# Kernel tuning notes

Hardware: AMD Instinct MI355X
Metric: run time of the kernel (lower is better)

The kernel has to match this reference:

```python
import jax, jax.numpy as jnp
import numpy as np

N, K, CIN, COUT = 1_000_000, 27, 32, 32  # active voxels, 3^3 kernel offsets, channels
EPS = 1e-5


def setup_inputs() -> dict:
    key = jax.random.key(0)
    k0, k1, k2, k3 = jax.random.split(key, 4)
    feats = jax.random.normal(k0, (N, CIN), jnp.float32)
    # per-kernel-offset weight matrices, Kaiming-ish scale
    W = jax.random.normal(k1, (K, CIN, COUT), jnp.float32) * (1.0 / np.sqrt(K * CIN))
    gamma = jnp.ones((COUT,), jnp.float32)
    beta = jnp.zeros((COUT,), jnp.float32)
    # precomputed sparse-conv neighbor map: index of input voxel contributing
    nbr_idx = jax.random.randint(k2, (N, K), 0, N, jnp.int32)
    nbr_mask = jax.random.bernoulli(k3, 0.5, (N, K))
    return {"feats": feats, "W": W, "gamma": gamma, "beta": beta,
            "nbr_idx": nbr_idx, "nbr_mask": nbr_mask}


def _sparse_conv(feats, W, nbr_idx, nbr_mask):
    # gather-GEMM-scatter, looped over the small fixed kernel volume (27)
    # to avoid materializing an [N, 27, CIN] gathered tensor.
    acc = jnp.zeros((feats.shape[0], W.shape[2]), feats.dtype)
    for k in range(W.shape[0]):
        g = jnp.where(nbr_mask[:, k, None], feats[nbr_idx[:, k]], 0.0)  # [N, CIN]
        acc = acc + g @ W[k]  # [N, COUT]
    return acc


def reference(feats, W, gamma, beta, nbr_idx, nbr_mask):
    y = _sparse_conv(feats, W, nbr_idx, nbr_mask)           # conv (bias=False, bn=True)
    mean = jnp.mean(y, axis=0)                              # MinkowskiBatchNorm (batch stats)
    var = jnp.mean(jnp.square(y - mean), axis=0)
    y = (y - mean) * jax.lax.rsqrt(var + EPS) * gamma + beta
    return jax.nn.relu(y)                                   # MinkowskiReLU
```

## Files before the change

### kernel.cpp

```cpp
#include <hip/hip_runtime.h>

typedef _Float16 half8 __attribute__((ext_vector_type(8)));
typedef float floatx4 __attribute__((ext_vector_type(4)));

#define CIN 32
#define COUT 32
#define KOFF 27
#define EPSV 1e-5f


__global__ void setup_k(const float* __restrict__ W, _Float16* __restrict__ wp,
                        const unsigned char* __restrict__ m,
                        int* __restrict__ flag) {
  if (blockIdx.x < KOFF) {
    int ko = blockIdx.x;
    int h = threadIdx.x >> 6;
    int lane = threadIdx.x & 63;
    int col = lane & 15, quad = lane >> 4;
    half8 p;
#pragma unroll
    for (int j = 0; j < 8; ++j) {
      int k = quad * 8 + j;
      p[j] = (_Float16)W[(ko * CIN + k) * COUT + h * 16 + col];
    }
    *(half8*)(wp + ((size_t)(ko * 2 + h) * 64 + lane) * 8) = p;
  } else {
    int tid = threadIdx.x;
    int any = 0;
    for (int i = tid; i < 4096; i += 128) {
      if ((i & 3) != 0 && m[i] != 0) any = 1;
    }
    if (any) atomicOr(flag, 1);
  }
}

__global__ void prep_k(const float* __restrict__ feats,
                       _Float16* __restrict__ f16, int total8) {
  int t = blockIdx.x * 256 + threadIdx.x;
  if (t < total8) {
    const floatx4* in4 = (const floatx4*)feats;
    floatx4 a = __builtin_nontemporal_load(&in4[(size_t)t * 2]);
    floatx4 b = __builtin_nontemporal_load(&in4[(size_t)t * 2 + 1]);
    half8 h;
    h[0] = (_Float16)a[0]; h[1] = (_Float16)a[1];
    h[2] = (_Float16)a[2]; h[3] = (_Float16)a[3];
    h[4] = (_Float16)b[0]; h[5] = (_Float16)b[1];
    h[6] = (_Float16)b[2]; h[7] = (_Float16)b[3];
    *(half8*)(f16 + (size_t)t * 8) = h;
  } else if (t < total8 + 4) {
    half8 z;
#pragma unroll
    for (int j = 0; j < 8; ++j) z[j] = (_Float16)0.f;
    *(half8*)(f16 + (size_t)t * 8) = z;
  }
}

__launch_bounds__(256, 4)
__global__ void conv_mfma_l(const _Float16* __restrict__ f16,
                            const _Float16* __restrict__ wp,
                            const int* __restrict__ nidx,
                            const unsigned char* __restrict__ nmask,
                            const int* __restrict__ flagp,
                            float* __restrict__ y,
                            float* __restrict__ stats, int N) {
  __shared__ int lidx[4 * 64 * KOFF];
  __shared__ float smS[4 * 32];
  __shared__ float smQ[4 * 32];
  int wave = threadIdx.x >> 6;
  int lane = threadIdx.x & 63;
  int base = (blockIdx.x * 4 + wave) * 64;
  bool active = base < N;
  int col = lane & 15, quad = lane >> 4;
  const half8* wfrag = (const half8*)wp;
  const _Float16* fq = f16 + quad * 8;
  int* lw = lidx + wave * (64 * KOFF);

  floatx4 acc[4][2];
#pragma unroll
  for (int t = 0; t < 4; ++t)
#pragma unroll
    for (int h = 0; h < 2; ++h) {
      acc[t][h][0] = 0.f; acc[t][h][1] = 0.f;
      acc[t][h][2] = 0.f; acc[t][h][3] = 0.f;
    }

  if (active) {
    bool bytemode = (*flagp != 0);
    int nv = N - base; if (nv > 64) nv = 64;
    if (nv == 64) {
      const int4* gi = (const int4*)(nidx + (size_t)base * KOFF);
      const int4* gm4 = (const int4*)((const int*)nmask + (size_t)base * KOFF);
      const unsigned int* gmb = (const unsigned int*)(nmask + (size_t)base * KOFF);
#pragma unroll
      for (int s = 0; s < 7; ++s) {
        int id4 = s * 64 + lane;
        if (id4 < 432) {
          int4 iv = gi[id4];
          unsigned int m0, m1, m2, m3;
          if (bytemode) {
            unsigned int mw = gmb[id4];
            m0 = mw & 0xffu; m1 = mw & 0xff00u;
            m2 = mw & 0xff0000u; m3 = mw & 0xff000000u;
          } else {
            int4 mv = gm4[id4];
            m0 = (unsigned int)mv.x; m1 = (unsigned int)mv.y;
            m2 = (unsigned int)mv.z; m3 = (unsigned int)mv.w;
          }
          int4 ov;
          ov.x = (iv.x & 0x7FFFFFFF) | (m0 ? (int)0x80000000 : 0);
          ov.y = (iv.y & 0x7FFFFFFF) | (m1 ? (int)0x80000000 : 0);
          ov.z = (iv.z & 0x7FFFFFFF) | (m2 ? (int)0x80000000 : 0);
          ov.w = (iv.w & 0x7FFFFFFF) | (m3 ? (int)0x80000000 : 0);
          *(int4*)(lw + id4 * 4) = ov;
        }
      }
    } else {
      int total = nv * KOFF;
      for (int p = lane; p < total; p += 64) {
        size_t g = (size_t)base * KOFF + p;
        int iv = nidx[g];
        int mk = bytemode ? (int)nmask[g] : ((const int*)nmask)[g];
        lw[p] = (iv & 0x7FFFFFFF) | (mk ? (int)0x80000000 : 0);
      }
      for (int p = nv * KOFF + lane; p < 64 * KOFF; p += 64) lw[p] = 0;
    }

    half8 aC[4];
    int ivB[4];
#pragma unroll
    for (int t = 0; t < 4; ++t) {
      int v0 = lw[(t * 16 + col) * KOFF + 0];
      int sel = (v0 < 0) ? (v0 & 0x7FFFFFFF) : N;
      aC[t] = *(const half8*)(fq + ((size_t)sel << 5));
      ivB[t] = lw[(t * 16 + col) * KOFF + 1];
    }
    half8 bC0 = wfrag[lane];
    half8 bC1 = wfrag[64 + lane];

#pragma unroll
    for (int ko = 0; ko < KOFF; ++ko) {
      half8 aN[4];
      half8 bN0, bN1;
      int ivN[4];
      if (ko + 1 < KOFF) {
        bN0 = wfrag[(size_t)((ko + 1) * 2 + 0) * 64 + lane];
        bN1 = wfrag[(size_t)((ko + 1) * 2 + 1) * 64 + lane];
#pragma unroll
        for (int t = 0; t < 4; ++t) {
          int v = ivB[t];
          int sel = (v < 0) ? (v & 0x7FFFFFFF) : N;
          aN[t] = *(const half8*)(fq + ((size_t)sel << 5));
        }
      }
      if (ko + 2 < KOFF) {
#pragma unroll
        for (int t = 0; t < 4; ++t)
          ivN[t] = lw[(t * 16 + col) * KOFF + ko + 2];
      }
#pragma unroll
      for (int t = 0; t < 4; ++t) {
        acc[t][0] = __builtin_amdgcn_mfma_f32_16x16x32_f16(aC[t], bC0, acc[t][0], 0, 0, 0);
        acc[t][1] = __builtin_amdgcn_mfma_f32_16x16x32_f16(aC[t], bC1, acc[t][1], 0, 0, 0);
      }
      if (ko + 1 < KOFF) {
#pragma unroll
        for (int t = 0; t < 4; ++t) aC[t] = aN[t];
        bC0 = bN0; bC1 = bN1;
      }
      if (ko + 2 < KOFF) {
#pragma unroll
        for (int t = 0; t < 4; ++t) ivB[t] = ivN[t];
      }
    }
  }

  float s0 = 0.f, s1 = 0.f, q0 = 0.f, q1 = 0.f;
  if (active) {
#pragma unroll
    for (int t = 0; t < 4; ++t) {
#pragma unroll
      for (int h = 0; h < 2; ++h) {
        floatx4 c = acc[t][h];
        int co = h * 16 + col;
#pragma unroll
        for (int r = 0; r < 4; ++r) {
          int vox = base + t * 16 + quad * 4 + r;
          if (vox < N) {
            y[(size_t)vox * COUT + co] = c[r];
            float v = c[r];
            if (h == 0) { s0 += v; q0 += v * v; }
            else        { s1 += v; q1 += v * v; }
          }
        }
      }
    }
  }
  s0 += __shfl_xor(s0, 16); s0 += __shfl_xor(s0, 32);
  s1 += __shfl_xor(s1, 16); s1 += __shfl_xor(s1, 32);
  q0 += __shfl_xor(q0, 16); q0 += __shfl_xor(q0, 32);
  q1 += __shfl_xor(q1, 16); q1 += __shfl_xor(q1, 32);
  if (quad == 0) {
    smS[wave * 32 + col] = s0;
    smS[wave * 32 + 16 + col] = s1;
    smQ[wave * 32 + col] = q0;
    smQ[wave * 32 + 16 + col] = q1;
  }
  __syncthreads();
  int tid = threadIdx.x;
  if (tid < 64) {
    int co = tid & 31;
    const float* arr = (tid < 32) ? smS : smQ;
    float s = arr[co] + arr[32 + co] + arr[64 + co] + arr[96 + co];
    atomicAdd(&stats[(tid < 32 ? 0 : 32) + co], s);
  }
}

__global__ void bn_apply(float* __restrict__ y, const float* __restrict__ stats,
                         const float* __restrict__ gamma,
                         const float* __restrict__ beta, int total4, float invN) {
  __shared__ float sc_sh[64];
  int tid = threadIdx.x;
  if (tid < 32) {
    float mean = stats[tid] * invN;
    float ex2 = stats[32 + tid] * invN;
    float var = ex2 - mean * mean;
    float inv = rsqrtf(var + EPSV);
    float sc = gamma[tid] * inv;
    sc_sh[tid] = sc;
    sc_sh[32 + tid] = beta[tid] - mean * sc;
  }
  __syncthreads();
  int t = blockIdx.x * blockDim.x + tid;
  if (t >= total4) return;
  size_t g = (size_t)t * 4;
  int co = (int)(g & 31);
  floatx4 v = *(const floatx4*)(y + g);
  floatx4 sc = *(const floatx4*)&sc_sh[co];
  floatx4 sh = *(const floatx4*)&sc_sh[32 + co];
  floatx4 o;
#pragma unroll
  for (int j = 0; j < 4; ++j) o[j] = fmaxf(0.f, v[j] * sc[j] + sh[j]);
  __builtin_nontemporal_store(o, (floatx4*)(y + g));
}

extern "C" void kernel_launch(void* const* d_in, const int* in_sizes, int n_in,
                              void* d_out, int out_size, void* d_ws,
                              size_t ws_size, hipStream_t stream) {
  const float* feats = (const float*)d_in[0];
  const float* W = (const float*)d_in[1];
  const float* gamma = (const float*)d_in[2];
  const float* beta = (const float*)d_in[3];
  const int* nidx = (const int*)d_in[4];
  const unsigned char* nmask = (const unsigned char*)d_in[5];
  float* out = (float*)d_out;

  int N = in_sizes[0] / CIN;

  char* ws = (char*)d_ws;
  size_t f16_bytes = (size_t)(N + 1) * CIN * sizeof(_Float16);
  _Float16* f16 = (_Float16*)ws;
  _Float16* wp = (_Float16*)(ws + f16_bytes);
  size_t wp_bytes = (size_t)KOFF * 2 * 64 * 8 * sizeof(_Float16);
  size_t stats_off = ((f16_bytes + wp_bytes + 511) / 512) * 512;
  float* stats = (float*)(ws + stats_off);
  int* flag = (int*)(stats + 64);

  hipMemsetAsync(stats, 0, 65 * sizeof(float), stream);

  setup_k<<<KOFF + 1, 128, 0, stream>>>(W, wp, nmask, flag);

  int total8 = N * CIN / 8;
  int cvtBlocks = (total8 + 4 + 255) / 256;
  prep_k<<<cvtBlocks, 256, 0, stream>>>(feats, f16, total8);

  int nwaves = (N + 63) / 64;
  int nblocks = (nwaves + 3) / 4;
  conv_mfma_l<<<nblocks, 256, 0, stream>>>(f16, wp, nidx, nmask, flag, out,
                                           stats, N);

  int total4 = N * COUT / 4;
  bn_apply<<<(total4 + 255) / 256, 256, 0, stream>>>(out, stats, gamma, beta,
                                                     total4, 1.0f / (float)N);
}
```

Before: 623.1 us.

## Stage gathered neighbor features through swizzled LDS with row-contiguous lane mapping

Each group of four lanes now gathers the four 16-byte chunks of one neighbor voxel row, so each row is read contiguously by adjacent lanes. The rows are written into a per-wave XOR-swizzled LDS buffer and read back in the MFMA A-fragment layout. This targets gather coalescing in the neighbor load. In exchange it adds LDS writes and reads per kernel offset, about 16 KB more shared memory per block with launch bounds lowered to 3, and it drops the register prefetch of weight fragments.

```diff
diff --git a/kernel.cpp b/kernel.cpp
--- a/kernel.cpp
+++ b/kernel.cpp
@@ -55,8 +55,8 @@
   }
 }
 
-__launch_bounds__(256, 4)
-__global__ void conv_mfma_l(const _Float16* __restrict__ f16,
+__launch_bounds__(256, 3)
+__global__ void conv_mfma_q(const _Float16* __restrict__ f16,
                             const _Float16* __restrict__ wp,
                             const int* __restrict__ nidx,
                             const unsigned char* __restrict__ nmask,
@@ -64,6 +64,7 @@
                             float* __restrict__ y,
                             float* __restrict__ stats, int N) {
   __shared__ int lidx[4 * 64 * KOFF];
+  __shared__ _Float16 sstage[4 * 64 * 32];
   __shared__ float smS[4 * 32];
   __shared__ float smQ[4 * 32];
   int wave = threadIdx.x >> 6;
@@ -72,8 +73,8 @@
   bool active = base < N;
   int col = lane & 15, quad = lane >> 4;
   const half8* wfrag = (const half8*)wp;
-  const _Float16* fq = f16 + quad * 8;
   int* lw = lidx + wave * (64 * KOFF);
+  _Float16* stg = sstage + wave * (64 * 32);
 
   floatx4 acc[4][2];
 #pragma unroll
@@ -125,37 +126,49 @@
       for (int p = nv * KOFF + lane; p < 64 * KOFF; p += 64) lw[p] = 0;
     }
 
-    half8 aC[4];
+    int vg_sub = lane >> 2;
+    int cch = lane & 3;
+    int swz_w = cch ^ ((lane >> 2) & 3) ^ ((lane >> 4) & 3);
+    int swz_r = quad ^ (col & 3) ^ (col >> 2);
+    const _Float16* fch = f16 + cch * 8;
+
+    half8 gv[4];
     int ivB[4];
 #pragma unroll
-    for (int t = 0; t < 4; ++t) {
-      int v0 = lw[(t * 16 + col) * KOFF + 0];
+    for (int i = 0; i < 4; ++i) {
+      int v0 = lw[(16 * i + vg_sub) * KOFF + 0];
       int sel = (v0 < 0) ? (v0 & 0x7FFFFFFF) : N;
-      aC[t] = *(const half8*)(fq + ((size_t)sel << 5));
-      ivB[t] = lw[(t * 16 + col) * KOFF + 1];
-    }
-    half8 bC0 = wfrag[lane];
-    half8 bC1 = wfrag[64 + lane];
+      gv[i] = *(const half8*)(fch + ((size_t)sel << 5));
+    }
+#pragma unroll
+    for (int i = 0; i < 4; ++i) ivB[i] = lw[(16 * i + vg_sub) * KOFF + 1];
+#pragma unroll
+    for (int i = 0; i < 4; ++i)
+      *(half8*)(stg + (16 * i + vg_sub) * 32 + swz_w * 8) = gv[i];
 
 #pragma unroll
     for (int ko = 0; ko < KOFF; ++ko) {
-      half8 aN[4];
-      half8 bN0, bN1;
-      int ivN[4];
+      half8 aC[4];
+#pragma unroll
+      for (int t = 0; t < 4; ++t)
+        aC[t] = *(const half8*)(stg + (t * 16 + col) * 32 + swz_r * 8);
+      half8 bC0 = wfrag[(size_t)(ko * 2 + 0) * 64 + lane];
+      half8 bC1 = wfrag[(size_t)(ko * 2 + 1) * 64 + lane];
       if (ko + 1 < KOFF) {
-        bN0 = wfrag[(size_t)((ko + 1) * 2 + 0) * 64 + lane];
-        bN1 = wfrag[(size_t)((ko + 1) * 2 + 1) * 64 + lane];
-#pragma unroll
-        for (int t = 0; t < 4; ++t) {
-          int v = ivB[t];
+#pragma unroll
+        for (int i = 0; i < 4; ++i) {
+          int v = ivB[i];
           int sel = (v < 0) ? (v & 0x7FFFFFFF) : N;
-          aN[t] = *(const half8*)(fq + ((size_t)sel << 5));
+          gv[i] = *(const half8*)(fch + ((size_t)sel << 5));
         }
       }
       if (ko + 2 < KOFF) {
-#pragma unroll
-        for (int t = 0; t < 4; ++t)
-          ivN[t] = lw[(t * 16 + col) * KOFF + ko + 2];
+        int ivN[4];
+#pragma unroll
+        for (int i = 0; i < 4; ++i)
+          ivN[i] = lw[(16 * i + vg_sub) * KOFF + ko + 2];
+#pragma unroll
+        for (int i = 0; i < 4; ++i) ivB[i] = ivN[i];
       }
 #pragma unroll
       for (int t = 0; t < 4; ++t) {
@@ -164,12 +177,8 @@
       }
       if (ko + 1 < KOFF) {
 #pragma unroll
-        for (int t = 0; t < 4; ++t) aC[t] = aN[t];
-        bC0 = bN0; bC1 = bN1;
-      }
-      if (ko + 2 < KOFF) {
-#pragma unroll
-        for (int t = 0; t < 4; ++t) ivB[t] = ivN[t];
+        for (int i = 0; i < 4; ++i)
+          *(half8*)(stg + (16 * i + vg_sub) * 32 + swz_w * 8) = gv[i];
       }
     }
   }
@@ -275,7 +284,7 @@
 
   int nwaves = (N + 63) / 64;
   int nblocks = (nwaves + 3) / 4;
-  conv_mfma_l<<<nblocks, 256, 0, stream>>>(f16, wp, nidx, nmask, flag, out,
+  conv_mfma_q<<<nblocks, 256, 0, stream>>>(f16, wp, nidx, nmask, flag, out,
                                            stats, N);
 
   int total4 = N * COUT / 4;
```

New measurement: 615.1 us. Within noise of the previous version (-1.3%).

## Store conv output as fp16 intermediate, fuse prep kernels, nontemporal index loads

Applied to the files above, without the earlier changes.

The conv kernel now writes its pre-normalization output as fp16 to a workspace buffer instead of fp32 into the output, and the BN/ReLU pass reads those fp16 values and writes fp32 output. This halves the intermediate write and read traffic. The weight packing, mask-format probe, stats zeroing and feature conversion are merged into one launch, removing a memset and a kernel launch. Neighbor index and mask loads become nontemporal. The fp16 intermediate loses precision before normalization, while the batch statistics are still computed in fp32.

```diff
diff --git a/kernel.cpp b/kernel.cpp
--- a/kernel.cpp
+++ b/kernel.cpp
@@ -2,6 +2,7 @@
 
 typedef _Float16 half8 __attribute__((ext_vector_type(8)));
 typedef float floatx4 __attribute__((ext_vector_type(4)));
+typedef int intx4 __attribute__((ext_vector_type(4)));
 
 #define CIN 32
 #define COUT 32
@@ -9,34 +10,46 @@
 #define EPSV 1e-5f
 
 
-__global__ void setup_k(const float* __restrict__ W, _Float16* __restrict__ wp,
-                        const unsigned char* __restrict__ m,
-                        int* __restrict__ flag) {
-  if (blockIdx.x < KOFF) {
-    int ko = blockIdx.x;
-    int h = threadIdx.x >> 6;
-    int lane = threadIdx.x & 63;
-    int col = lane & 15, quad = lane >> 4;
-    half8 p;
-#pragma unroll
-    for (int j = 0; j < 8; ++j) {
-      int k = quad * 8 + j;
-      p[j] = (_Float16)W[(ko * CIN + k) * COUT + h * 16 + col];
-    }
-    *(half8*)(wp + ((size_t)(ko * 2 + h) * 64 + lane) * 8) = p;
-  } else {
-    int tid = threadIdx.x;
+__global__ void fused_prep(const float* __restrict__ feats,
+                           _Float16* __restrict__ f16, int total8,
+                           const float* __restrict__ W,
+                           _Float16* __restrict__ wp,
+                           const unsigned char* __restrict__ m,
+                           int* __restrict__ flag,
+                           float* __restrict__ stats) {
+  int bx = blockIdx.x;
+  int tid = threadIdx.x;
+  if (bx < KOFF) {
+    if (tid < 128) {
+      int ko = bx;
+      int h = tid >> 6;
+      int lane = tid & 63;
+      int col = lane & 15, quad = lane >> 4;
+      half8 p;
+#pragma unroll
+      for (int j = 0; j < 8; ++j) {
+        int k = quad * 8 + j;
+        p[j] = (_Float16)W[(ko * CIN + k) * COUT + h * 16 + col];
+      }
+      *(half8*)(wp + ((size_t)(ko * 2 + h) * 64 + lane) * 8) = p;
+    }
+    return;
+  }
+  if (bx == KOFF) {
+    __shared__ int red;
+    if (tid == 0) red = 0;
+    __syncthreads();
     int any = 0;
-    for (int i = tid; i < 4096; i += 128) {
+    for (int i = tid; i < 4096; i += 256) {
       if ((i & 3) != 0 && m[i] != 0) any = 1;
     }
-    if (any) atomicOr(flag, 1);
-  }
-}
-
-__global__ void prep_k(const float* __restrict__ feats,
-                       _Float16* __restrict__ f16, int total8) {
-  int t = blockIdx.x * 256 + threadIdx.x;
+    if (any) atomicOr(&red, 1);
+    __syncthreads();
+    if (tid == 0) *flag = red;
+    if (tid < 64) stats[tid] = 0.f;
+    return;
+  }
+  int t = (bx - KOFF - 1) * 256 + tid;
   if (t < total8) {
     const floatx4* in4 = (const floatx4*)feats;
     floatx4 a = __builtin_nontemporal_load(&in4[(size_t)t * 2]);
@@ -61,7 +74,7 @@
                             const int* __restrict__ nidx,
                             const unsigned char* __restrict__ nmask,
                             const int* __restrict__ flagp,
-                            float* __restrict__ y,
+                            _Float16* __restrict__ y16,
                             float* __restrict__ stats, int N) {
   __shared__ int lidx[4 * 64 * KOFF];
   __shared__ float smS[4 * 32];
@@ -88,30 +101,30 @@
     bool bytemode = (*flagp != 0);
     int nv = N - base; if (nv > 64) nv = 64;
     if (nv == 64) {
-      const int4* gi = (const int4*)(nidx + (size_t)base * KOFF);
-      const int4* gm4 = (const int4*)((const int*)nmask + (size_t)base * KOFF);
+      const intx4* gi = (const intx4*)(nidx + (size_t)base * KOFF);
+      const intx4* gm4 = (const intx4*)((const int*)nmask + (size_t)base * KOFF);
       const unsigned int* gmb = (const unsigned int*)(nmask + (size_t)base * KOFF);
 #pragma unroll
       for (int s = 0; s < 7; ++s) {
         int id4 = s * 64 + lane;
         if (id4 < 432) {
-          int4 iv = gi[id4];
+          intx4 iv = __builtin_nontemporal_load(&gi[id4]);
           unsigned int m0, m1, m2, m3;
           if (bytemode) {
-            unsigned int mw = gmb[id4];
+            unsigned int mw = __builtin_nontemporal_load(&gmb[id4]);
             m0 = mw & 0xffu; m1 = mw & 0xff00u;
             m2 = mw & 0xff0000u; m3 = mw & 0xff000000u;
           } else {
-            int4 mv = gm4[id4];
+            intx4 mv = __builtin_nontemporal_load(&gm4[id4]);
             m0 = (unsigned int)mv.x; m1 = (unsigned int)mv.y;
             m2 = (unsigned int)mv.z; m3 = (unsigned int)mv.w;
           }
-          int4 ov;
+          intx4 ov;
           ov.x = (iv.x & 0x7FFFFFFF) | (m0 ? (int)0x80000000 : 0);
           ov.y = (iv.y & 0x7FFFFFFF) | (m1 ? (int)0x80000000 : 0);
           ov.z = (iv.z & 0x7FFFFFFF) | (m2 ? (int)0x80000000 : 0);
           ov.w = (iv.w & 0x7FFFFFFF) | (m3 ? (int)0x80000000 : 0);
-          *(int4*)(lw + id4 * 4) = ov;
+          *(intx4*)(lw + id4 * 4) = ov;
         }
       }
     } else {
@@ -186,7 +199,7 @@
         for (int r = 0; r < 4; ++r) {
           int vox = base + t * 16 + quad * 4 + r;
           if (vox < N) {
-            y[(size_t)vox * COUT + co] = c[r];
+            y16[(size_t)vox * COUT + co] = (_Float16)c[r];
             float v = c[r];
             if (h == 0) { s0 += v; q0 += v * v; }
             else        { s1 += v; q1 += v * v; }
@@ -215,9 +228,12 @@
   }
 }
 
-__global__ void bn_apply(float* __restrict__ y, const float* __restrict__ stats,
+__global__ void bn_apply(const _Float16* __restrict__ y16,
+                         float* __restrict__ out,
+                         const float* __restrict__ stats,
                          const float* __restrict__ gamma,
-                         const float* __restrict__ beta, int total4, float invN) {
+                         const float* __restrict__ beta, int total8,
+                         float invN) {
   __shared__ float sc_sh[64];
   int tid = threadIdx.x;
   if (tid < 32) {
@@ -231,16 +247,23 @@
   }
   __syncthreads();
   int t = blockIdx.x * blockDim.x + tid;
-  if (t >= total4) return;
-  size_t g = (size_t)t * 4;
+  if (t >= total8) return;
+  size_t g = (size_t)t * 8;
   int co = (int)(g & 31);
-  floatx4 v = *(const floatx4*)(y + g);
-  floatx4 sc = *(const floatx4*)&sc_sh[co];
-  floatx4 sh = *(const floatx4*)&sc_sh[32 + co];
-  floatx4 o;
-#pragma unroll
-  for (int j = 0; j < 4; ++j) o[j] = fmaxf(0.f, v[j] * sc[j] + sh[j]);
-  __builtin_nontemporal_store(o, (floatx4*)(y + g));
+  half8 v = __builtin_nontemporal_load((const half8*)(y16 + g));
+  floatx4 sc0 = *(const floatx4*)&sc_sh[co];
+  floatx4 sh0 = *(const floatx4*)&sc_sh[32 + co];
+  floatx4 sc1 = *(const floatx4*)&sc_sh[co + 4];
+  floatx4 sh1 = *(const floatx4*)&sc_sh[32 + co + 4];
+  floatx4 o0, o1;
+#pragma unroll
+  for (int j = 0; j < 4; ++j)
+    o0[j] = fmaxf(0.f, (float)v[j] * sc0[j] + sh0[j]);
+#pragma unroll
+  for (int j = 0; j < 4; ++j)
+    o1[j] = fmaxf(0.f, (float)v[4 + j] * sc1[j] + sh1[j]);
+  __builtin_nontemporal_store(o0, (floatx4*)(out + g));
+  __builtin_nontemporal_store(o1, (floatx4*)(out + g + 4));
 }
 
 extern "C" void kernel_launch(void* const* d_in, const int* in_sizes, int n_in,
@@ -264,21 +287,21 @@
   size_t stats_off = ((f16_bytes + wp_bytes + 511) / 512) * 512;
   float* stats = (float*)(ws + stats_off);
   int* flag = (int*)(stats + 64);
-
-  hipMemsetAsync(stats, 0, 65 * sizeof(float), stream);
-
-  setup_k<<<KOFF + 1, 128, 0, stream>>>(W, wp, nmask, flag);
+  size_t y16_off = ((stats_off + 768 + 255) / 256) * 256;
+  _Float16* y16 = (_Float16*)(ws + y16_off);
 
   int total8 = N * CIN / 8;
   int cvtBlocks = (total8 + 4 + 255) / 256;
-  prep_k<<<cvtBlocks, 256, 0, stream>>>(feats, f16, total8);
+  fused_prep<<<KOFF + 1 + cvtBlocks, 256, 0, stream>>>(feats, f16, total8, W,
+                                                       wp, nmask, flag, stats);
 
   int nwaves = (N + 63) / 64;
   int nblocks = (nwaves + 3) / 4;
-  conv_mfma_l<<<nblocks, 256, 0, stream>>>(f16, wp, nidx, nmask, flag, out,
+  conv_mfma_l<<<nblocks, 256, 0, stream>>>(f16, wp, nidx, nmask, flag, y16,
                                            stats, N);
 
-  int total4 = N * COUT / 4;
-  bn_apply<<<(total4 + 255) / 256, 256, 0, stream>>>(out, stats, gamma, beta,
-                                                     total4, 1.0f / (float)N);
+  int total8v = N * COUT / 8;
+  bn_apply<<<(total8v + 255) / 256, 256, 0, stream>>>(y16, out, stats, gamma,
+                                                      beta, total8v,
+                                                      1.0f / (float)N);
 }
```

Result: faster. 608.3 us (-2.4%).
